# Optimization experiments

Measured on AMD Instinct MI355X. Metric: run time of the kernel, lower is better.

## Reference

```python
import jax, jax.numpy as jnp
import numpy as np

# --- constants mirroring init_kwargs ---
DIM = 1024
N_HEADS = 16
N_KV_HEADS = 4
HEAD_DIM = DIM // N_HEADS          # 64
REP = N_HEADS // N_KV_HEADS        # 4
ROPE_THETA = 10000.0
WINDOW = 512
N_GLOBAL = 64
EPS = 1e-6


def setup_inputs() -> dict:
    key = jax.random.key(0)
    ks = jax.random.split(key, 7)
    B, L = 2, 2048
    x = jax.random.normal(ks[0], (B, L, DIM), dtype=jnp.float32)
    s = 0.02
    wq = jax.random.normal(ks[1], (DIM, N_HEADS * HEAD_DIM), dtype=jnp.float32) * s
    wk = jax.random.normal(ks[2], (DIM, N_KV_HEADS * HEAD_DIM), dtype=jnp.float32) * s
    wv = jax.random.normal(ks[3], (DIM, N_KV_HEADS * HEAD_DIM), dtype=jnp.float32) * s
    wo = jax.random.normal(ks[4], (N_HEADS * HEAD_DIM, DIM), dtype=jnp.float32) * s
    gq = jnp.ones((HEAD_DIM,), dtype=jnp.float32) + 0.01 * jax.random.normal(ks[5], (HEAD_DIM,), dtype=jnp.float32)
    gk = jnp.ones((HEAD_DIM,), dtype=jnp.float32) + 0.01 * jax.random.normal(ks[6], (HEAD_DIM,), dtype=jnp.float32)
    return {"x": x, "wq": wq, "wk": wk, "wv": wv, "wo": wo, "gq": gq, "gk": gk}


def _rmsnorm(t, g):
    # QKNorm: RMS norm over head_dim with learnable per-dim scale
    return t * jax.lax.rsqrt(jnp.mean(t * t, axis=-1, keepdims=True) + EPS) * g


def _rope(t, cos, sin):
    # t: [B,H,L,hd]; complex RoPE over consecutive pairs (2i, 2i+1)
    t1 = t[..., 0::2]
    t2 = t[..., 1::2]
    o1 = t1 * cos - t2 * sin
    o2 = t1 * sin + t2 * cos
    return jnp.stack([o1, o2], axis=-1).reshape(t.shape)


def reference(x, wq, wk, wv, wo, gq, gk):
    B, L, D = x.shape
    q = (x @ wq).reshape(B, L, N_HEADS, HEAD_DIM)
    k = (x @ wk).reshape(B, L, N_KV_HEADS, HEAD_DIM)
    v = (x @ wv).reshape(B, L, N_KV_HEADS, HEAD_DIM)
    q = _rmsnorm(q, gq)
    k = _rmsnorm(k, gk)
    q = q.transpose(0, 2, 1, 3)  # [B,H,L,hd]
    k = k.transpose(0, 2, 1, 3)
    v = v.transpose(0, 2, 1, 3)

    # RoPE frequencies (start_pos = 0)
    inv_freq = 1.0 / (ROPE_THETA ** (jnp.arange(0, HEAD_DIM, 2, dtype=jnp.float32) / HEAD_DIM))
    ang = jnp.arange(L, dtype=jnp.float32)[:, None] * inv_freq[None, :]  # [L, hd/2]
    cos, sin = jnp.cos(ang), jnp.sin(ang)
    q = _rope(q, cos, sin)
    k = _rope(k, cos, sin)

    # GQA: repeat kv heads (repeat_interleave on head dim)
    k = jnp.repeat(k, REP, axis=1)
    v = jnp.repeat(v, REP, axis=1)

    scores = jnp.einsum("bhqd,bhkd->bhqk", q, k) / np.sqrt(HEAD_DIM).astype(np.float32)

    # sliding-window + global-token causal mask
    half = WINDOW // 2
    i = jnp.arange(L)[:, None]
    j = jnp.arange(L)[None, :]
    m = (j <= i) & ((j >= i - half) | (j < N_GLOBAL))  # [L,L] bool
    scores = jnp.where(m[None, None], scores, -jnp.inf)

    attn = jax.nn.softmax(scores.astype(jnp.float32), axis=-1).astype(scores.dtype)
    out = jnp.einsum("bhqk,bhkd->bhqd", attn, v)
    out = out.transpose(0, 2, 1, 3).reshape(B, L, N_HEADS * HEAD_DIM)
    return out @ wo
```

## Files before the change

kernel.cpp:

```cpp
#include <hip/hip_runtime.h>
#include <hip/hip_bf16.h>

typedef __bf16 bf16x8 __attribute__((ext_vector_type(8)));
typedef __bf16 bf16x4 __attribute__((ext_vector_type(4)));
typedef float  f32x4  __attribute__((ext_vector_type(4)));
typedef short  s16x4  __attribute__((ext_vector_type(4)));

__device__ __forceinline__ __bf16 to_bf16(float f) {
    __hip_bfloat16 h = __float2bfloat16(f);
    return *reinterpret_cast<__bf16*>(&h);
}

__device__ __forceinline__ f32x4 mfma32(bf16x8 a, bf16x8 b, f32x4 c) {
    return __builtin_amdgcn_mfma_f32_16x16x32_bf16(a, b, c, 0, 0, 0);
}
__device__ __forceinline__ f32x4 mfma16(bf16x4 a, bf16x4 b, f32x4 c) {
#if __has_builtin(__builtin_amdgcn_mfma_f32_16x16x16_bf16)
    return __builtin_amdgcn_mfma_f32_16x16x16_bf16(a, b, c, 0, 0, 0);
#else
    return __builtin_amdgcn_mfma_f32_16x16x16bf16_1k(
        __builtin_bit_cast(s16x4, a), __builtin_bit_cast(s16x4, b), c, 0, 0, 0);
#endif
}

__device__ __forceinline__ void gload_lds16(const __bf16* g, __bf16* l) {
    __builtin_amdgcn_global_load_lds(
        (const __attribute__((address_space(1))) void*)g,
        (__attribute__((address_space(3))) void*)l, 16, 0, 0);
}


__global__ __launch_bounds__(256) void prep_k(const float* __restrict__ wq,
                                              const float* __restrict__ wk,
                                              const float* __restrict__ wv,
                                              const float* __restrict__ wo,
                                              const float* __restrict__ x,
                                              __bf16* __restrict__ WqkvT,
                                              __bf16* __restrict__ WoT,
                                              __bf16* __restrict__ xb,
                                              float2* __restrict__ rope_tab) {
    int b = blockIdx.x, tid = threadIdx.x;
    if (b >= 4608) {
        int idx = (b - 4608) * 256 + tid;
        int pos = idx >> 5, f = idx & 31;
        float ex = (float)(2 * f) * (1.0f / 64.0f);
        float invf = expf(-ex * 9.210340371976184f);
        float ang = (float)pos * invf;
        rope_tab[idx] = make_float2(cosf(ang), sinf(ang));
        return;
    }
    if (b >= 2560) {
        int i = ((b - 2560) * 256 + tid) * 8;
        f32x4 a = *(const f32x4*)(x + i);
        f32x4 c = *(const f32x4*)(x + i + 4);
        bf16x8 h;
        h[0] = to_bf16(a.x); h[1] = to_bf16(a.y); h[2] = to_bf16(a.z); h[3] = to_bf16(a.w);
        h[4] = to_bf16(c.x); h[5] = to_bf16(c.y); h[6] = to_bf16(c.z); h[7] = to_bf16(c.w);
        *(bf16x8*)(xb + i) = h;
        return;
    }
    __shared__ float tile[32][33];
    const float* src; __bf16* dst; int N, idx;
    if (b < 1024)      { src = wq; dst = WqkvT;                        N = 1024; idx = b; }
    else if (b < 1280) { src = wk; dst = WqkvT + (size_t)1024 * 1024;  N = 256;  idx = b - 1024; }
    else if (b < 1536) { src = wv; dst = WqkvT + (size_t)1280 * 1024;  N = 256;  idx = b - 1280; }
    else               { src = wo; dst = WoT;                          N = 1024; idx = b - 1536; }
    int k0 = (idx & 31) * 32, n0 = (idx >> 5) * 32;
    int tx = tid & 31, ty = tid >> 5;
#pragma unroll
    for (int r = 0; r < 4; ++r) {
        int kk = ty + r * 8;
        tile[kk][tx] = src[(size_t)(k0 + kk) * N + n0 + tx];
    }
    __syncthreads();
#pragma unroll
    for (int r = 0; r < 4; ++r) {
        int nn = ty + r * 8;
        dst[(size_t)(n0 + nn) * 1024 + k0 + tx] = to_bf16(tile[tx][nn]);
    }
}

#define GEMM_CORE128(A, BT, K)                                                  \
    __shared__ __bf16 smem[16384];                                              \
    __bf16* lA = smem;                                                          \
    __bf16* lB = smem + 8192;                                                   \
    int tid = threadIdx.x;                                                      \
    int m0 = blockIdx.x * 128, n0 = blockIdx.y * 128;                           \
    int wid = tid >> 6, lane = tid & 63;                                        \
    int wm = (wid & 1) * 64, wn = (wid >> 1) * 64;                              \
    int lm = lane & 15, qd = lane >> 4;                                         \
    f32x4 acc[4][4] = {};                                                       \
    for (int k0 = 0; k0 < (K); k0 += 64) {                                      \
        _Pragma("unroll")                                                       \
        for (int it = 0; it < 4; ++it) {                                        \
            int kh = it >> 1, half = it & 1;                                    \
            int c = half * 256 + tid;                                           \
            int row = c >> 2, c4 = c & 3;                                       \
            __bf16* ldst = lA + kh * 4096 + half * 2048 + wid * 512;            \
            gload_lds16((A) + (size_t)(m0 + row) * (K) + k0 + kh * 32 + c4 * 8, ldst); \
            __bf16* ldstb = lB + kh * 4096 + half * 2048 + wid * 512;           \
            gload_lds16((BT) + (size_t)(n0 + row) * (K) + k0 + kh * 32 + c4 * 8, ldstb); \
        }                                                                       \
        __syncthreads();                                                        \
        _Pragma("unroll")                                                       \
        for (int kh = 0; kh < 2; ++kh) {                                        \
            bf16x8 af[4], bfr[4];                                               \
            _Pragma("unroll")                                                   \
            for (int t = 0; t < 4; ++t) {                                       \
                int row = wm + t * 16 + lm;                                     \
                af[t] = *(const bf16x8*)&lA[kh * 4096 + (row >> 6) * 2048       \
                                            + (row & 63) * 32 + qd * 8];        \
                int col = wn + t * 16 + lm;                                     \
                bfr[t] = *(const bf16x8*)&lB[kh * 4096 + (col >> 6) * 2048      \
                                             + (col & 63) * 32 + qd * 8];       \
            }                                                                   \
            _Pragma("unroll")                                                   \
            for (int ti = 0; ti < 4; ++ti)                                      \
                _Pragma("unroll")                                               \
                for (int tj = 0; tj < 4; ++tj)                                  \
                    acc[ti][tj] = mfma32(af[ti], bfr[tj], acc[ti][tj]);         \
        }                                                                       \
        __syncthreads();                                                        \
    }

__global__ __launch_bounds__(256) void gemmqkv_k(const __bf16* __restrict__ A,
                                                 const __bf16* __restrict__ BT,
                                                 const float2* __restrict__ rope_tab,
                                                 const float* __restrict__ gq,
                                                 const float* __restrict__ gk,
                                                 __bf16* __restrict__ Qb,
                                                 __bf16* __restrict__ Kbl,
                                                 __bf16* __restrict__ Vt) {
    GEMM_CORE128(A, BT, 1024)
    int head0 = n0 >> 6;

    if (head0 < 20) {
        int head = head0 + (wn >> 6);
        bool isq = head < 16;
        const float* gvec = isq ? gq : gk;
        float gam[4];
#pragma unroll
        for (int tj = 0; tj < 4; ++tj) gam[tj] = gvec[tj * 16 + lm];
#pragma unroll
        for (int ti = 0; ti < 4; ++ti)
#pragma unroll
            for (int r = 0; r < 4; ++r) {
                int row = wm + ti * 16 + qd * 4 + r;
                int t = m0 + row;
                int pos = t & 2047, bb = t >> 11;
                float ss = acc[ti][0][r] * acc[ti][0][r] + acc[ti][1][r] * acc[ti][1][r]
                         + acc[ti][2][r] * acc[ti][2][r] + acc[ti][3][r] * acc[ti][3][r];
                ss += __shfl_xor(ss, 1);
                ss += __shfl_xor(ss, 2);
                ss += __shfl_xor(ss, 4);
                ss += __shfl_xor(ss, 8);
                float scale = rsqrtf(ss * (1.0f / 64.0f) + 1e-6f);
#pragma unroll
                for (int tj = 0; tj < 4; ++tj) {
                    int cw = tj * 16 + lm;
                    float v = acc[ti][tj][r] * scale * gam[tj];
                    float2 cs = rope_tab[pos * 32 + (cw >> 1)];
                    float pv = __shfl_xor(v, 1);
                    float outv = (cw & 1) ? (pv * cs.y + v * cs.x) : (v * cs.x - pv * cs.y);
                    if (isq) {
                        int kvh = head >> 2, h4 = head & 3;
                        size_t off = (((((size_t)bb * 4 + kvh) * 128 + (pos >> 4)) * 4 + h4) * 16
                                      + (pos & 15)) * 64 + cw;
                        Qb[off] = to_bf16(outv * 0.125f);
                    } else {
                        int kvg = head - 16;
                        Kbl[(((size_t)bb * 4 + kvg) * 2048 + pos) * 64 + cw] = to_bf16(outv);
                    }
                }
            }
    } else {
        __bf16* tv = smem;
        int bb = m0 >> 11, pos0 = m0 & 2047;
#pragma unroll
        for (int hh = 0; hh < 2; ++hh) {
            if ((wn >> 6) == hh) {
#pragma unroll
                for (int ti = 0; ti < 4; ++ti)
#pragma unroll
                    for (int tj = 0; tj < 4; ++tj)
#pragma unroll
                        for (int r = 0; r < 4; ++r) {
                            int row = wm + ti * 16 + qd * 4 + r;
                            int cw = tj * 16 + lm;
                            tv[cw * 136 + row] = to_bf16(acc[ti][tj][r]);
                        }
            }
            __syncthreads();
            int kvg = head0 + hh - 20;
            size_t gg = (size_t)bb * 4 + kvg;
#pragma unroll
            for (int p = 0; p < 4; ++p) {
                int d = p * 16 + (tid >> 4);
                int tok = (tid & 15) * 8;
                bf16x8 vvv = *(const bf16x8*)&tv[d * 136 + tok];
                *(bf16x8*)(Vt + (gg * 64 + d) * 2048 + pos0 + tok) = vvv;
            }
            __syncthreads();
        }
    }
}

__global__ __launch_bounds__(256) void gemm_bf16_k(const __bf16* __restrict__ A,
                                                   const __bf16* __restrict__ BT,
                                                   float* __restrict__ C,
                                                   int K, int N) {
    GEMM_CORE128(A, BT, K)
#pragma unroll
    for (int ti = 0; ti < 4; ++ti)
#pragma unroll
        for (int tj = 0; tj < 4; ++tj)
#pragma unroll
            for (int r = 0; r < 4; ++r) {
                int row = m0 + wm + ti * 16 + qd * 4 + r;
                int col = n0 + wn + tj * 16 + lm;
                C[(size_t)row * N + col] = acc[ti][tj][r];
            }
}

__global__ __launch_bounds__(512) void attn_k(const __bf16* __restrict__ Qb,
                                              const __bf16* __restrict__ Kbl,
                                              const __bf16* __restrict__ Vt,
                                              __bf16* __restrict__ aout) {
    __shared__ __bf16 Kt[2][64 * 64];
    __shared__ __bf16 Vl[2][64 * 64];
    int tid = threadIdx.x, wid = tid >> 6, lane = tid & 63;
    int l15 = lane & 15, quad = lane >> 4;
    int qb = blockIdx.x, kvh = blockIdx.y, b = blockIdx.z;
    int qg = wid >> 2;
    int h4 = wid & 3;
    int iw0 = qb * 32;
    int iw = iw0 + qg * 16;
    int g = b * 4 + kvh;
    int h = kvh * 4 + h4;
    int e7 = l15 & 7;

    int qbi = qb * 2 + qg;
    const __bf16* qp = Qb + ((((size_t)g * 128 + qbi) * 4 + h4) * 16 + l15) * 64 + quad * 8;
    bf16x8 qf0 = *(const bf16x8*)qp;
    bf16x8 qf1 = *(const bf16x8*)(qp + 32);

    int ts = (iw0 - 256) >> 6; if (ts < 1) ts = 1;
    int tmaxb = (iw0 + 31) >> 6;
    int n_all = (tmaxb >= ts) ? (tmaxb - ts + 2) : 1;
    int tmaxw = (iw + 15) >> 6;

    const __bf16* Kg = Kbl + (size_t)g * 2048 * 64;
    const __bf16* Vg = Vt + (size_t)g * 64 * 2048;

    int r0 = tid >> 3, c0 = tid & 7;
    int kl = r0 * 64 + ((c0 ^ (r0 & 7)) * 8);

    bf16x8 kr, vr;
    auto stage_load = [&](int tt) {
        kr = *(const bf16x8*)(Kg + (size_t)tt * 64 * 64 + r0 * 64 + c0 * 8);
        vr = *(const bf16x8*)(Vg + (size_t)r0 * 2048 + tt * 64 + c0 * 8);
    };
    auto stage_write = [&](int buf) {
        *(bf16x8*)&Kt[buf][kl] = kr;
        *(bf16x8*)&Vl[buf][kl] = vr;
    };

    stage_load(0);
    stage_write(0);

    f32x4 o[4] = {};
    float mr = -1e30f, lrp = 0.f;
    int iq = iw + l15;

    for (int idx = 0; idx < n_all; ++idx) {
        int tt = (idx == 0) ? 0 : ts + idx - 1;
        if (idx + 1 < n_all) stage_load(ts + idx);
        __syncthreads();
        int buf = idx & 1;

        f32x4 s[4] = {};
#pragma unroll
        for (int nt = 0; nt < 4; ++nt) {
            const __bf16* kp = &Kt[buf][(nt * 16 + l15) * 64];
            bf16x8 k0 = *(const bf16x8*)(kp + ((quad ^ e7) * 8));
            bf16x8 k1 = *(const bf16x8*)(kp + (((quad + 4) ^ e7) * 8));
            s[nt] = mfma32(k0, qf0, s[nt]);
            s[nt] = mfma32(k1, qf1, s[nt]);
        }

        bool need_mask = (tt >= tmaxw) || (tt >= 1 && tt * 64 < iw + 15 - 256);
        if (need_mask) {
#pragma unroll
            for (int nt = 0; nt < 4; ++nt)
#pragma unroll
                for (int r = 0; r < 4; ++r) {
                    int j = tt * 64 + nt * 16 + quad * 4 + r;
                    bool valid = (j <= iq) && ((j >= iq - 256) || (j < 64));
                    s[nt][r] = valid ? s[nt][r] : -1e30f;
                }
        }

        float mx = -1e30f;
#pragma unroll
        for (int nt = 0; nt < 4; ++nt)
#pragma unroll
            for (int r = 0; r < 4; ++r) mx = fmaxf(mx, s[nt][r]);
        mx = fmaxf(mx, __shfl_xor(mx, 16));
        mx = fmaxf(mx, __shfl_xor(mx, 32));
        float mn = fmaxf(mr, mx);
        float alpha = __expf(mr - mn);
        mr = mn;

        float ps = 0.f;
        bf16x4 pb[4];
#pragma unroll
        for (int nt = 0; nt < 4; ++nt)
#pragma unroll
            for (int r = 0; r < 4; ++r) {
                float pv = __expf(s[nt][r] - mn);
                ps += pv;
                pb[nt][r] = to_bf16(pv);
            }
        lrp = lrp * alpha + ps;

#pragma unroll
        for (int dt = 0; dt < 4; ++dt) {
            o[dt] *= alpha;
            const __bf16* vp = &Vl[buf][(dt * 16 + l15) * 64];
#pragma unroll
            for (int nt = 0; nt < 4; ++nt) {
                int c8 = 2 * nt + (quad >> 1);
                bf16x4 va = *(const bf16x4*)(vp + ((c8 ^ e7) * 8) + (quad & 1) * 4);
                o[dt] = mfma16(va, pb[nt], o[dt]);
            }
        }

        if (idx + 1 < n_all) stage_write((idx + 1) & 1);
    }

    lrp += __shfl_xor(lrp, 16);
    lrp += __shfl_xor(lrp, 32);
    float inv = 1.f / lrp;
    __syncthreads();
    __bf16* pr = (__bf16*)Kt + wid * 16 * 64;
#pragma unroll
    for (int dt = 0; dt < 4; ++dt)
#pragma unroll
        for (int r = 0; r < 4; ++r) {
            int e = dt * 16 + quad * 4 + r;
            int c8 = e >> 3;
            pr[l15 * 64 + ((c8 ^ e7) * 8) + (e & 7)] = to_bf16(o[dt][r] * inv);
        }
    bf16x8 o0 = *(const bf16x8*)(pr + l15 * 64 + (((2 * quad) ^ e7) * 8));
    bf16x8 o1 = *(const bf16x8*)(pr + l15 * 64 + (((2 * quad + 1) ^ e7) * 8));
    __bf16* op = aout + ((size_t)b * 2048 + iw + l15) * 1024 + h * 64 + quad * 16;
    *(bf16x8*)op = o0;
    *(bf16x8*)(op + 8) = o1;
}

extern "C" void kernel_launch(void* const* d_in, const int* in_sizes, int n_in,
                              void* d_out, int out_size, void* d_ws, size_t ws_size,
                              hipStream_t stream) {
    const float* x  = (const float*)d_in[0];
    const float* wq = (const float*)d_in[1];
    const float* wk = (const float*)d_in[2];
    const float* wv = (const float*)d_in[3];
    const float* wo = (const float*)d_in[4];
    const float* gq = (const float*)d_in[5];
    const float* gk = (const float*)d_in[6];
    float* out = (float*)d_out;

    char* ws = (char*)d_ws;
    __bf16*  WqkvT = (__bf16*)ws;
    __bf16*  WoT   = (__bf16*)(ws + 3145728);
    __bf16*  xb_ao = (__bf16*)(ws + 5242880);
    __bf16*  Kbl   = (__bf16*)(ws + 13631488);
    __bf16*  Vt    = (__bf16*)(ws + 15728640);
    __bf16*  Qb    = (__bf16*)(ws + 17825792);
    float2*  rtab  = (float2*)(ws + 26214400);

    dim3 tb(256);
    prep_k<<<4864, tb, 0, stream>>>(wq, wk, wv, wo, x, WqkvT, WoT, xb_ao, rtab);
    gemmqkv_k<<<dim3(32, 12), tb, 0, stream>>>(xb_ao, WqkvT, rtab, gq, gk, Qb, Kbl, Vt);
    attn_k<<<dim3(64, 4, 2), dim3(512), 0, stream>>>(Qb, Kbl, Vt, xb_ao);
    gemm_bf16_k<<<dim3(32, 8), tb, 0, stream>>>(xb_ao, WoT, out, 1024, 1024);
}
```

Measured before the change: 148.4 us.

## Double-buffer GEMM LDS tiles and split 128x128 tile across eight waves

The shared GEMM core now double-buffers the A/B tiles in LDS, issuing the next k-slice's global-to-LDS loads before computing the current one, with explicit vmcnt waits and raw barriers replacing the two syncthreads per iteration. Blocks grow from 256 to 512 threads, so each wave computes a 64x32 sub-tile instead of 64x64, and the QKV epilogue now reduces RMS-norm sums across wave pairs through a small shared buffer. The V transpose writes both heads at once. This is meant to hide global load latency and raise per-CU wave count, at the cost of twice the LDS per block and an extra barrier in the epilogue.

```diff
diff --git a/kernel.cpp b/kernel.cpp
--- a/kernel.cpp
+++ b/kernel.cpp
@@ -81,49 +81,62 @@
 }
 
 #define GEMM_CORE128(A, BT, K)                                                  \
-    __shared__ __bf16 smem[16384];                                              \
-    __bf16* lA = smem;                                                          \
-    __bf16* lB = smem + 8192;                                                   \
+    __shared__ __bf16 smem[32768];                                              \
     int tid = threadIdx.x;                                                      \
     int m0 = blockIdx.x * 128, n0 = blockIdx.y * 128;                           \
     int wid = tid >> 6, lane = tid & 63;                                        \
-    int wm = (wid & 1) * 64, wn = (wid >> 1) * 64;                              \
+    int wm = (wid & 1) * 64, wn = (wid >> 1) * 32;                              \
     int lm = lane & 15, qd = lane >> 4;                                         \
-    f32x4 acc[4][4] = {};                                                       \
-    for (int k0 = 0; k0 < (K); k0 += 64) {                                      \
+    int srow = tid >> 2, sc4 = tid & 3;                                         \
+    f32x4 acc[4][2] = {};                                                       \
+    int nt = (K) / 64;                                                          \
+    auto STAGE = [&](int bsel, int t) {                                         \
+        __bf16* base = smem + bsel * 16384;                                     \
         _Pragma("unroll")                                                       \
-        for (int it = 0; it < 4; ++it) {                                        \
-            int kh = it >> 1, half = it & 1;                                    \
-            int c = half * 256 + tid;                                           \
-            int row = c >> 2, c4 = c & 3;                                       \
-            __bf16* ldst = lA + kh * 4096 + half * 2048 + wid * 512;            \
-            gload_lds16((A) + (size_t)(m0 + row) * (K) + k0 + kh * 32 + c4 * 8, ldst); \
-            __bf16* ldstb = lB + kh * 4096 + half * 2048 + wid * 512;           \
-            gload_lds16((BT) + (size_t)(n0 + row) * (K) + k0 + kh * 32 + c4 * 8, ldstb); \
+        for (int kh = 0; kh < 2; ++kh)                                          \
+            gload_lds16((A) + (size_t)(m0 + srow) * (K) + t * 64 + kh * 32 + sc4 * 8, \
+                        base + kh * 4096 + wid * 512);                          \
+        _Pragma("unroll")                                                       \
+        for (int kh = 0; kh < 2; ++kh)                                          \
+            gload_lds16((BT) + (size_t)(n0 + srow) * (K) + t * 64 + kh * 32 + sc4 * 8, \
+                        base + 8192 + kh * 4096 + wid * 512);                   \
+    };                                                                          \
+    STAGE(0, 0);                                                                \
+    for (int t = 0; t < nt; ++t) {                                              \
+        if (t + 1 < nt) {                                                       \
+            STAGE((t + 1) & 1, t + 1);                                          \
+            asm volatile("s_waitcnt vmcnt(4)" ::: "memory");                    \
+        } else {                                                                \
+            asm volatile("s_waitcnt vmcnt(0)" ::: "memory");                    \
         }                                                                       \
-        __syncthreads();                                                        \
+        __builtin_amdgcn_s_barrier();                                           \
+        __builtin_amdgcn_sched_barrier(0);                                      \
+        const __bf16* cA = smem + (t & 1) * 16384;                              \
+        const __bf16* cB = cA + 8192;                                           \
         _Pragma("unroll")                                                       \
         for (int kh = 0; kh < 2; ++kh) {                                        \
-            bf16x8 af[4], bfr[4];                                               \
+            bf16x8 af[4], bfr[2];                                               \
             _Pragma("unroll")                                                   \
-            for (int t = 0; t < 4; ++t) {                                       \
-                int row = wm + t * 16 + lm;                                     \
-                af[t] = *(const bf16x8*)&lA[kh * 4096 + (row >> 6) * 2048       \
-                                            + (row & 63) * 32 + qd * 8];        \
-                int col = wn + t * 16 + lm;                                     \
-                bfr[t] = *(const bf16x8*)&lB[kh * 4096 + (col >> 6) * 2048      \
-                                             + (col & 63) * 32 + qd * 8];       \
+            for (int t4 = 0; t4 < 4; ++t4) {                                    \
+                int row = wm + t4 * 16 + lm;                                    \
+                af[t4] = *(const bf16x8*)&cA[kh * 4096 + row * 32 + qd * 8];    \
+            }                                                                   \
+            _Pragma("unroll")                                                   \
+            for (int j = 0; j < 2; ++j) {                                       \
+                int col = wn + j * 16 + lm;                                     \
+                bfr[j] = *(const bf16x8*)&cB[kh * 4096 + col * 32 + qd * 8];    \
             }                                                                   \
             _Pragma("unroll")                                                   \
             for (int ti = 0; ti < 4; ++ti)                                      \
                 _Pragma("unroll")                                               \
-                for (int tj = 0; tj < 4; ++tj)                                  \
+                for (int tj = 0; tj < 2; ++tj)                                  \
                     acc[ti][tj] = mfma32(af[ti], bfr[tj], acc[ti][tj]);         \
         }                                                                       \
-        __syncthreads();                                                        \
-    }
-
-__global__ __launch_bounds__(256) void gemmqkv_k(const __bf16* __restrict__ A,
+        asm volatile("s_waitcnt lgkmcnt(0)" ::: "memory");                      \
+        __builtin_amdgcn_s_barrier();                                           \
+    }
+
+__global__ __launch_bounds__(512) void gemmqkv_k(const __bf16* __restrict__ A,
                                                  const __bf16* __restrict__ BT,
                                                  const float2* __restrict__ rope_tab,
                                                  const float* __restrict__ gq,
@@ -131,16 +144,33 @@
                                                  __bf16* __restrict__ Qb,
                                                  __bf16* __restrict__ Kbl,
                                                  __bf16* __restrict__ Vt) {
+    __shared__ float ssp[4][128];
     GEMM_CORE128(A, BT, 1024)
     int head0 = n0 >> 6;
+    int quad = wid >> 1;
+    int chead = wn & 63;
 
     if (head0 < 20) {
-        int head = head0 + (wn >> 6);
+        int head = head0 + (quad >> 1);
         bool isq = head < 16;
         const float* gvec = isq ? gq : gk;
-        float gam[4];
-#pragma unroll
-        for (int tj = 0; tj < 4; ++tj) gam[tj] = gvec[tj * 16 + lm];
+        float gam[2];
+#pragma unroll
+        for (int tj = 0; tj < 2; ++tj) gam[tj] = gvec[chead + tj * 16 + lm];
+
+#pragma unroll
+        for (int ti = 0; ti < 4; ++ti)
+#pragma unroll
+            for (int r = 0; r < 4; ++r) {
+                float sq = acc[ti][0][r] * acc[ti][0][r] + acc[ti][1][r] * acc[ti][1][r];
+                sq += __shfl_xor(sq, 1);
+                sq += __shfl_xor(sq, 2);
+                sq += __shfl_xor(sq, 4);
+                sq += __shfl_xor(sq, 8);
+                if (lm == 0) ssp[quad][wm + ti * 16 + qd * 4 + r] = sq;
+            }
+        __syncthreads();
+
 #pragma unroll
         for (int ti = 0; ti < 4; ++ti)
 #pragma unroll
@@ -148,16 +178,11 @@
                 int row = wm + ti * 16 + qd * 4 + r;
                 int t = m0 + row;
                 int pos = t & 2047, bb = t >> 11;
-                float ss = acc[ti][0][r] * acc[ti][0][r] + acc[ti][1][r] * acc[ti][1][r]
-                         + acc[ti][2][r] * acc[ti][2][r] + acc[ti][3][r] * acc[ti][3][r];
-                ss += __shfl_xor(ss, 1);
-                ss += __shfl_xor(ss, 2);
-                ss += __shfl_xor(ss, 4);
-                ss += __shfl_xor(ss, 8);
+                float ss = ssp[quad][row] + ssp[quad ^ 1][row];
                 float scale = rsqrtf(ss * (1.0f / 64.0f) + 1e-6f);
 #pragma unroll
-                for (int tj = 0; tj < 4; ++tj) {
-                    int cw = tj * 16 + lm;
+                for (int tj = 0; tj < 2; ++tj) {
+                    int cw = chead + tj * 16 + lm;
                     float v = acc[ti][tj][r] * scale * gam[tj];
                     float2 cs = rope_tab[pos * 32 + (cw >> 1)];
                     float pv = __shfl_xor(v, 1);
@@ -174,38 +199,34 @@
                 }
             }
     } else {
-        __bf16* tv = smem;
+        __bf16* tvh = smem + (quad >> 1) * 8704;
         int bb = m0 >> 11, pos0 = m0 & 2047;
 #pragma unroll
-        for (int hh = 0; hh < 2; ++hh) {
-            if ((wn >> 6) == hh) {
-#pragma unroll
-                for (int ti = 0; ti < 4; ++ti)
-#pragma unroll
-                    for (int tj = 0; tj < 4; ++tj)
-#pragma unroll
-                        for (int r = 0; r < 4; ++r) {
-                            int row = wm + ti * 16 + qd * 4 + r;
-                            int cw = tj * 16 + lm;
-                            tv[cw * 136 + row] = to_bf16(acc[ti][tj][r]);
-                        }
-            }
-            __syncthreads();
-            int kvg = head0 + hh - 20;
-            size_t gg = (size_t)bb * 4 + kvg;
-#pragma unroll
-            for (int p = 0; p < 4; ++p) {
-                int d = p * 16 + (tid >> 4);
-                int tok = (tid & 15) * 8;
-                bf16x8 vvv = *(const bf16x8*)&tv[d * 136 + tok];
-                *(bf16x8*)(Vt + (gg * 64 + d) * 2048 + pos0 + tok) = vvv;
-            }
-            __syncthreads();
+        for (int ti = 0; ti < 4; ++ti)
+#pragma unroll
+            for (int tj = 0; tj < 2; ++tj)
+#pragma unroll
+                for (int r = 0; r < 4; ++r) {
+                    int row = wm + ti * 16 + qd * 4 + r;
+                    int cw = chead + tj * 16 + lm;
+                    tvh[cw * 136 + row] = to_bf16(acc[ti][tj][r]);
+                }
+        __syncthreads();
+        int hh = tid >> 8, t8 = tid & 255;
+        int kvg = head0 + hh - 20;
+        size_t gg = (size_t)bb * 4 + kvg;
+        const __bf16* tvr = smem + hh * 8704;
+#pragma unroll
+        for (int p = 0; p < 4; ++p) {
+            int d = p * 16 + (t8 >> 4);
+            int tok = (t8 & 15) * 8;
+            bf16x8 vvv = *(const bf16x8*)&tvr[d * 136 + tok];
+            *(bf16x8*)(Vt + (gg * 64 + d) * 2048 + pos0 + tok) = vvv;
         }
     }
 }
 
-__global__ __launch_bounds__(256) void gemm_bf16_k(const __bf16* __restrict__ A,
+__global__ __launch_bounds__(512) void gemm_bf16_k(const __bf16* __restrict__ A,
                                                    const __bf16* __restrict__ BT,
                                                    float* __restrict__ C,
                                                    int K, int N) {
@@ -213,7 +234,7 @@
 #pragma unroll
     for (int ti = 0; ti < 4; ++ti)
 #pragma unroll
-        for (int tj = 0; tj < 4; ++tj)
+        for (int tj = 0; tj < 2; ++tj)
 #pragma unroll
             for (int r = 0; r < 4; ++r) {
                 int row = m0 + wm + ti * 16 + qd * 4 + r;
@@ -379,9 +400,8 @@
     __bf16*  Qb    = (__bf16*)(ws + 17825792);
     float2*  rtab  = (float2*)(ws + 26214400);
 
-    dim3 tb(256);
-    prep_k<<<4864, tb, 0, stream>>>(wq, wk, wv, wo, x, WqkvT, WoT, xb_ao, rtab);
-    gemmqkv_k<<<dim3(32, 12), tb, 0, stream>>>(xb_ao, WqkvT, rtab, gq, gk, Qb, Kbl, Vt);
+    prep_k<<<4864, dim3(256), 0, stream>>>(wq, wk, wv, wo, x, WqkvT, WoT, xb_ao, rtab);
+    gemmqkv_k<<<dim3(32, 12), dim3(512), 0, stream>>>(xb_ao, WqkvT, rtab, gq, gk, Qb, Kbl, Vt);
     attn_k<<<dim3(64, 4, 2), dim3(512), 0, stream>>>(Qb, Kbl, Vt, xb_ao);
-    gemm_bf16_k<<<dim3(32, 8), tb, 0, stream>>>(xb_ao, WoT, out, 1024, 1024);
-}
+    gemm_bf16_k<<<dim3(32, 8), dim3(512), 0, stream>>>(xb_ao, WoT, out, 1024, 1024);
+}
```

Measured after the change: 140.0 us. 5.7% less time.
